# Performance work log

Hardware: AMD Instinct MI355X
Metric: run time of the kernel (lower is better)

## Reference

```python
import jax, jax.numpy as jnp
import numpy as np
from jax import lax

B = 8192; LE = 40; LD = 12; PQ = 237; IN = PQ + 19; H = 64


def setup_inputs() -> dict:
    key = jax.random.key(0)
    ks = jax.random.split(key, 26)
    def n(k, shape, s=0.05):
        return jax.random.normal(k, shape, jnp.float32) * s
    return {
        "input_p_q": jax.random.normal(ks[0], (B, LE, PQ), jnp.float32),
        "label_p": jax.random.normal(ks[1], (B, LE), jnp.float32),
        "emb_hour": n(ks[2], (24, 5)),
        "emb_weekday": n(ks[3], (8, 3)),
        "emb_month": n(ks[4], (13, 4)),
        "emb_woy": n(ks[5], (54, 7)),
        "Wi_w": n(ks[6], (H, IN)), "Wi_b": n(ks[7], (H,)),
        "We_w": n(ks[8], (H, 2 * H)),
        "Vd_w": n(ks[9], (IN, H)), "Vd_b": n(ks[10], (IN,)),
        "enc_Wih": n(ks[11], (4 * H, IN)), "enc_Whh": n(ks[12], (4 * H, H)),
        "enc_bih": n(ks[13], (4 * H,)), "enc_bhh": n(ks[14], (4 * H,)),
        "Wd_w": n(ks[15], (H, H)), "Wd_b": n(ks[16], (H,)),
        "Wd2_w": n(ks[17], (H, 2)),
        "Vdt_w": n(ks[18], (1, H)), "Vdt_b": n(ks[19], (1,)),
        "dec_Wih": n(ks[20], (4, H + 1)), "dec_Whh": n(ks[21], (4, 1)),
        "dec_bih": n(ks[22], (4,)), "dec_bhh": n(ks[23], (4,)),
        "input_time": jax.random.randint(ks[24], (B, LE, 4), 0, 8),
        "decoder_time": jax.random.randint(ks[25], (B, LD), 0, 24),
    }


def _lstm_cell(x, h, c, Wih, Whh, bih, bhh):
    # PyTorch LSTMCell gate order: i, f, g, o
    g = x @ Wih.T + bih + h @ Whh.T + bhh
    i, f, gg, o = jnp.split(g, 4, axis=1)
    c = jax.nn.sigmoid(f) * c + jax.nn.sigmoid(i) * jnp.tanh(gg)
    h = jax.nn.sigmoid(o) * jnp.tanh(c)
    return h, c


def _forward(input_p_q, label_p, emb_hour, emb_weekday, emb_month, emb_woy,
             Wi_w, Wi_b, We_w, Vd_w, Vd_b,
             enc_Wih, enc_Whh, enc_bih, enc_bhh,
             Wd_w, Wd_b, Wd2_w, Vdt_w, Vdt_b,
             dec_Wih, dec_Whh, dec_bih, dec_bhh, input_time):
    b = input_p_q.shape[0]
    inputs = jnp.concatenate([
        input_p_q,
        emb_hour[input_time[:, :, 0]],
        emb_weekday[input_time[:, :, 1]],
        emb_month[input_time[:, :, 2]],
        emb_woy[input_time[:, :, 3]],
    ], axis=2)  # [B, LE, IN]

    def enc_step(carry, x_t):
        h, c = carry
        score = jnp.tanh(jnp.concatenate([h, c], 1) @ We_w.T
                         + x_t @ Wi_w.T + Wi_b) @ Vd_w.T + Vd_b  # [B, IN]
        x_in = x_t * jax.nn.softmax(score, axis=1)
        h, c = _lstm_cell(x_in, h, c, enc_Wih, enc_Whh, enc_bih, enc_bhh)
        return (h, c), h

    z = jnp.zeros((b, H), inputs.dtype)
    _, mid = lax.scan(enc_step, (z, z), jnp.swapaxes(inputs, 0, 1))
    mid_output = jnp.swapaxes(mid, 0, 1)  # [B, LE, H]

    wd_mid = mid_output @ Wd_w.T + Wd_b  # precompute Wd(mid_output), [B, LE, H]
    dec_p_in = label_p[:, LE - 1:LE]  # [B, 1], held constant across decode steps

    def dec_step(carry, _):
        hi, ci = carry  # [B, 1] each
        q = jnp.concatenate([hi, ci], 1) @ Wd2_w.T  # [B, H]
        score = jnp.tanh(q[:, None, :] + wd_mid) @ Vdt_w.T + Vdt_b  # [B, LE, 1] (no softmax, as in source)
        ctx = jnp.einsum('bt,btd->bd', score[..., 0], mid_output)  # [B, H]
        hi, ci = _lstm_cell(jnp.concatenate([ctx, dec_p_in], 1), hi, ci,
                            dec_Wih, dec_Whh, dec_bih, dec_bhh)
        return (hi, ci), hi

    z1 = jnp.zeros((b, 1), inputs.dtype)
    _, outs = lax.scan(dec_step, (z1, z1), None, length=LD)  # [LD, B, 1]
    return jnp.swapaxes(outs[..., 0], 0, 1)  # [B, LD]


def reference(input_p_q, label_p, emb_hour, emb_weekday, emb_month, emb_woy,
              Wi_w, Wi_b, We_w, Vd_w, Vd_b,
              enc_Wih, enc_Whh, enc_bih, enc_bhh,
              Wd_w, Wd_b, Wd2_w, Vdt_w, Vdt_b,
              dec_Wih, dec_Whh, dec_bih, dec_bhh, input_time, decoder_time):
    # decoder_time is accepted by the original forward but never used
    return _forward(input_p_q, label_p, emb_hour, emb_weekday, emb_month, emb_woy,
                    Wi_w, Wi_b, We_w, Vd_w, Vd_b,
                    enc_Wih, enc_Whh, enc_bih, enc_bhh,
                    Wd_w, Wd_b, Wd2_w, Vdt_w, Vdt_b,
                    dec_Wih, dec_Whh, dec_bih, dec_bhh, input_time)
```

## Files before the change

kernel.cpp:

```cpp
#include <hip/hip_runtime.h>

#define BB   8192
#define LEN  40
#define LDN  12
#define PQN  237
#define INN  256
#define HN   64
#define BT   32
#define ENC_BLOCKS (BB / BT)
#define DW   8
#define DEC_BLOCKS (BB / DW)
#define XPS  256

typedef unsigned int  u32;
typedef _Float16 f16;
typedef f16  half8 __attribute__((ext_vector_type(8)));
typedef f16  f16x4 __attribute__((ext_vector_type(4)));
typedef float f32x4 __attribute__((ext_vector_type(4)));

#define XS 264
#define HS 72

#define OFF_WI   0
#define OFF_WE   16384
#define OFF_VD   24576
#define OFF_WIH  40960
#define OFF_WHH  106496
#define OFF_WD   122880
#define W_TOTAL  126976

#define T_H   0
#define T_W   120
#define T_M   144
#define T_Y   196
#define T_TOT 574

#define PREP_BLOCKS (BB * LEN / 32)
#define CONV_BLOCKS ((W_TOTAL + 255) / 256)

__device__ __forceinline__ float rcp_(float x){
#if __has_builtin(__builtin_amdgcn_rcpf)
  return __builtin_amdgcn_rcpf(x);
#else
  return 1.0f / x;
#endif
}
__device__ __forceinline__ float sigm(float x){
  return rcp_(1.0f + exp2f(-1.44269504f * x));
}
__device__ __forceinline__ float tanhf_(float x){
  float e = exp2f(2.88539008f * x);
  return 1.0f - 2.0f * rcp_(e + 1.0f);
}

__device__ __forceinline__ void bar_lds(){
  asm volatile("s_waitcnt lgkmcnt(0)" ::: "memory");
  __builtin_amdgcn_s_barrier();
  asm volatile("" ::: "memory");
}

__global__ __launch_bounds__(256) void conv_w(
    const float* __restrict__ Wi, const float* __restrict__ We,
    const float* __restrict__ Vd, const float* __restrict__ Wih,
    const float* __restrict__ Whh, const float* __restrict__ Wd,
    f16* __restrict__ dst)
{
  int i = blockIdx.x * 256 + threadIdx.x;
  if (i >= W_TOTAL) return;
  float v;
  if      (i < OFF_WE)  v = Wi [i - OFF_WI ];
  else if (i < OFF_VD)  v = We [i - OFF_WE ];
  else if (i < OFF_WIH) v = Vd [i - OFF_VD ];
  else if (i < OFF_WHH) v = Wih[i - OFF_WIH];
  else if (i < OFF_WD)  v = Whh[i - OFF_WHH];
  else                  v = Wd [i - OFF_WD ];
  dst[i] = (f16)v;
}

__global__ __launch_bounds__(256) void prep_all(
    const float* __restrict__ ipq,
    const float* __restrict__ e_h, const float* __restrict__ e_w,
    const float* __restrict__ e_m, const float* __restrict__ e_y,
    const int*  __restrict__ itime,
    f16* __restrict__ xpre,
    const float* __restrict__ Wi, const float* __restrict__ We,
    const float* __restrict__ Vd, const float* __restrict__ Wih,
    const float* __restrict__ Whh, const float* __restrict__ Wd,
    f16* __restrict__ wdst)
{
  if (blockIdx.x >= PREP_BLOCKS) {
    int i = (blockIdx.x - PREP_BLOCKS) * 256 + threadIdx.x;
    if (i >= W_TOTAL) return;
    float v;
    if      (i < OFF_WE)  v = Wi [i - OFF_WI ];
    else if (i < OFF_VD)  v = We [i - OFF_WE ];
    else if (i < OFF_WIH) v = Vd [i - OFF_VD ];
    else if (i < OFF_WHH) v = Wih[i - OFF_WIH];
    else if (i < OFF_WD)  v = Whh[i - OFF_WHH];
    else                  v = Wd [i - OFF_WD ];
    wdst[i] = (f16)v;
    return;
  }
  const int wv = threadIdx.x >> 6, l = threadIdx.x & 63;
  const size_t row0 = (size_t)blockIdx.x * 32 + (size_t)wv * 8;
  int4 itv[8];
  #pragma unroll
  for (int r = 0; r < 8; ++r)
    itv[r] = *(const int4*)(itime + (row0 + r) * 4);
  #pragma unroll
  for (int r = 0; r < 8; ++r) {
    const size_t row = row0 + r;
    const float* src = ipq + row * PQN;
    f16* dst = xpre + row * XPS;
    #pragma unroll
    for (int k = 0; k < 3; ++k) {
      const int c = k * 64 + l;
      dst[c] = (f16)src[c];
    }
    {
      const int c = 192 + l;
      float v;
      if (c < PQN) v = src[c];
      else {
        const int o = c - PQN;
        if      (o < 5 ) v = e_h[itv[r].x * 5 + o];
        else if (o < 8 ) v = e_w[itv[r].y * 3 + (o - 5)];
        else if (o < 12) v = e_m[itv[r].z * 4 + (o - 8)];
        else             v = e_y[itv[r].w * 7 + (o - 12)];
      }
      dst[c] = (f16)v;
    }
  }
}

__global__ __launch_bounds__(256, 1) void enc_x(
    const f16* __restrict__ xpre,
    const float* __restrict__ Wi_b,
    const float* __restrict__ Vd_b,
    const float* __restrict__ ebih, const float* __restrict__ ebhh,
    const float* __restrict__ Wd_b,
    const f16*  __restrict__ wAll,
    f16* __restrict__ xout)
{
  __shared__ __attribute__((aligned(16))) f16 Xl[2][BT * XS];
  __shared__ __attribute__((aligned(16))) f16 Ul[BT * HS];
  __shared__ __attribute__((aligned(16))) f16 Hl[2][BT * HS];
  __shared__ __attribute__((aligned(16))) f16 Cl[2][BT * HS];
  __shared__ __attribute__((aligned(16))) f16 Wml[BT * HS];
  __shared__ float Sred[2 * 64];

  const int tid  = threadIdx.x;
  const int w    = tid >> 6;
  const int lane = tid & 63;
  const int nl   = lane & 15;
  const int q    = lane >> 4;
  const int b0   = blockIdx.x * BT;
  const int d0   = w * 16 + q * 4;

  const int r0  = tid >> 5;
  const int off = tid & 31;
  const f16* gb = xpre + ((size_t)(b0 + r0) * LEN) * XPS + off * 8;
  const u32 lw0 = (u32)(r0 * XS + off * 8);

  const int orow = tid >> 3;
  const int oc8  = (tid & 7) * 8;

  half8 sr[4];
  #pragma unroll
  for (int j = 0; j < 4; ++j)
    sr[j] = *(const half8*)(gb + (size_t)(8 * j) * LEN * XPS);

  half8 wif[8], wef[4], vdf[4][2], whf[4][8], whhf[4][2], wdf[2];
  {
    const f16* pw = wAll + OFF_WI + (w * 16 + nl) * 256 + q * 8;
    #pragma unroll
    for (int kt = 0; kt < 8; ++kt) wif[kt] = *(const half8*)(pw + kt * 32);
    const f16* pe = wAll + OFF_WE + (w * 16 + nl) * 128 + q * 8;
    #pragma unroll
    for (int kt = 0; kt < 4; ++kt) wef[kt] = *(const half8*)(pe + kt * 32);
    #pragma unroll
    for (int i = 0; i < 4; ++i) {
      const f16* pv = wAll + OFF_VD + ((w + 4*i) * 16 + nl) * 64 + q * 8;
      #pragma unroll
      for (int kt = 0; kt < 2; ++kt) vdf[i][kt] = *(const half8*)(pv + kt * 32);
      const f16* ph = wAll + OFF_WIH + ((w + 4*i) * 16 + nl) * 256 + q * 8;
      #pragma unroll
      for (int kt = 0; kt < 8; ++kt) whf[i][kt] = *(const half8*)(ph + kt * 32);
      const f16* pq = wAll + OFF_WHH + ((w + 4*i) * 16 + nl) * 64 + q * 8;
      #pragma unroll
      for (int kt = 0; kt < 2; ++kt) whhf[i][kt] = *(const half8*)(pq + kt * 32);
    }
    const f16* pd = wAll + OFF_WD + (w * 16 + nl) * 64 + q * 8;
    #pragma unroll
    for (int kt = 0; kt < 2; ++kt) wdf[kt] = *(const half8*)(pd + kt * 32);
  }

  float wib[4], vdb[16], ebs[16], wdb[4];
  #pragma unroll
  for (int r = 0; r < 4; ++r) { wib[r] = Wi_b[d0 + r]; wdb[r] = Wd_b[d0 + r]; }
  #pragma unroll
  for (int i = 0; i < 4; ++i)
    #pragma unroll
    for (int r = 0; r < 4; ++r) {
      vdb[i*4+r] = Vd_b[(w + 4*i) * 16 + q * 4 + r];
      ebs[i*4+r] = ebih[i * 64 + d0 + r] + ebhh[i * 64 + d0 + r];
    }

  for (int i = tid; i < BT * HS; i += 256) {
    Hl[0][i] = (f16)0.f; Cl[0][i] = (f16)0.f;
  }
  float creg[2][4];
  #pragma unroll
  for (int bt = 0; bt < 2; ++bt)
    #pragma unroll
    for (int r = 0; r < 4; ++r) creg[bt][r] = 0.f;
  bar_lds();

  for (int t = 0; t < LEN; ++t) {
    const int cur = t & 1, nxt = cur ^ 1;
    #pragma unroll
    for (int j = 0; j < 4; ++j)
      *(half8*)(&Xl[cur][lw0 + j * 8 * XS]) = sr[j];
    if (t + 1 < LEN) {
      const f16* gp = gb + (size_t)(t + 1) * XPS;
      #pragma unroll
      for (int j = 0; j < 4; ++j)
        sr[j] = *(const half8*)(gp + (size_t)(8 * j) * LEN * XPS);
    }
    bar_lds();

    #pragma unroll
    for (int bt = 0; bt < 2; ++bt) {
      const int row = bt * 16 + nl;
      f32x4 acc = {0.f, 0.f, 0.f, 0.f};
      const f16* xb = &Xl[cur][row * XS + q * 8];
      #pragma unroll
      for (int kt = 0; kt < 8; ++kt)
        acc = __builtin_amdgcn_mfma_f32_16x16x32_f16(wif[kt], *(const half8*)(xb + kt * 32), acc, 0, 0, 0);
      const f16* hb = &Hl[cur][row * HS + q * 8];
      const f16* cb = &Cl[cur][row * HS + q * 8];
      half8 h0 = *(const half8*)hb, h1 = *(const half8*)(hb + 32);
      half8 c0 = *(const half8*)cb, c1 = *(const half8*)(cb + 32);
      acc = __builtin_amdgcn_mfma_f32_16x16x32_f16(wef[0], h0, acc, 0, 0, 0);
      acc = __builtin_amdgcn_mfma_f32_16x16x32_f16(wef[1], h1, acc, 0, 0, 0);
      acc = __builtin_amdgcn_mfma_f32_16x16x32_f16(wef[2], c0, acc, 0, 0, 0);
      acc = __builtin_amdgcn_mfma_f32_16x16x32_f16(wef[3], c1, acc, 0, 0, 0);
      f16x4 uv;
      #pragma unroll
      for (int r = 0; r < 4; ++r) uv[r] = (f16)tanhf_(acc[r] + wib[r]);
      *(f16x4*)(&Ul[row * HS + d0]) = uv;
      if (t > 0) {
        f32x4 aw = {0.f, 0.f, 0.f, 0.f};
        aw = __builtin_amdgcn_mfma_f32_16x16x32_f16(wdf[0], h0, aw, 0, 0, 0);
        aw = __builtin_amdgcn_mfma_f32_16x16x32_f16(wdf[1], h1, aw, 0, 0, 0);
        f16x4 wv;
        #pragma unroll
        for (int r = 0; r < 4; ++r) wv[r] = (f16)(aw[r] + wdb[r]);
        *(f16x4*)(&Wml[row * HS + d0]) = wv;
      }
    }
    bar_lds();

    if (t > 0) {
      half8 hv8 = *(const half8*)(&Hl[cur][orow * HS + oc8]);
      half8 wv8 = *(const half8*)(&Wml[orow * HS + oc8]);
      f16* xr = xout + ((size_t)(b0 + orow) * LEN + (t - 1)) * XPS;
      *(half8*)(xr + oc8)      = hv8;
      *(half8*)(xr + 64 + oc8) = wv8;
    }
    #pragma unroll
    for (int bt = 0; bt < 2; ++bt) {
      const int row = bt * 16 + nl;
      const f16* ub = &Ul[row * HS + q * 8];
      half8 u0 = *(const half8*)ub, u1 = *(const half8*)(ub + 32);
      float ee[16];
      #pragma unroll
      for (int i = 0; i < 4; ++i) {
        f32x4 acc = {0.f, 0.f, 0.f, 0.f};
        acc = __builtin_amdgcn_mfma_f32_16x16x32_f16(vdf[i][0], u0, acc, 0, 0, 0);
        acc = __builtin_amdgcn_mfma_f32_16x16x32_f16(vdf[i][1], u1, acc, 0, 0, 0);
        #pragma unroll
        for (int r = 0; r < 4; ++r)
          ee[i*4+r] = exp2f((acc[r] + vdb[i*4+r]) * 1.44269504f);
      }
      float s = 0.f;
      #pragma unroll
      for (int j = 0; j < 16; ++j) s += ee[j];
      s += __shfl_xor(s, 16, 64);
      s += __shfl_xor(s, 32, 64);
      if (lane < 16) Sred[bt * 64 + w * 16 + lane] = s;
      #pragma unroll
      for (int i = 0; i < 4; ++i) {
        const int k = (w + 4*i) * 16 + q * 4;
        f16x4 xv = *(const f16x4*)(&Xl[cur][row * XS + k]);
        f16x4 pv;
        #pragma unroll
        for (int r = 0; r < 4; ++r) pv[r] = (f16)((float)xv[r] * ee[i*4+r]);
        *(f16x4*)(&Xl[cur][row * XS + k]) = pv;
      }
    }
    bar_lds();

    #pragma unroll
    for (int bt = 0; bt < 2; ++bt) {
      const int row = bt * 16 + nl;
      f32x4 g[4], gh[4];
      #pragma unroll
      for (int i = 0; i < 4; ++i) {
        g[i]  = (f32x4){0.f, 0.f, 0.f, 0.f};
        gh[i] = (f32x4){0.f, 0.f, 0.f, 0.f};
      }
      const f16* pb = &Xl[cur][row * XS + q * 8];
      #pragma unroll
      for (int kt = 0; kt < 8; ++kt) {
        half8 bv = *(const half8*)(pb + kt * 32);
        #pragma unroll
        for (int i = 0; i < 4; ++i)
          g[i] = __builtin_amdgcn_mfma_f32_16x16x32_f16(whf[i][kt], bv, g[i], 0, 0, 0);
      }
      const f16* hb = &Hl[cur][row * HS + q * 8];
      half8 h0 = *(const half8*)hb, h1 = *(const half8*)(hb + 32);
      #pragma unroll
      for (int i = 0; i < 4; ++i) {
        gh[i] = __builtin_amdgcn_mfma_f32_16x16x32_f16(whhf[i][0], h0, gh[i], 0, 0, 0);
        gh[i] = __builtin_amdgcn_mfma_f32_16x16x32_f16(whhf[i][1], h1, gh[i], 0, 0, 0);
      }
      const float inv = rcp_(Sred[bt*64 + nl]      + Sred[bt*64 + 16 + nl]
                           + Sred[bt*64 + 32 + nl] + Sred[bt*64 + 48 + nl]);
      f16x4 hv, cv;
      #pragma unroll
      for (int r = 0; r < 4; ++r) {
        const float gi = g[0][r] * inv + gh[0][r] + ebs[0  + r];
        const float gf = g[1][r] * inv + gh[1][r] + ebs[4  + r];
        const float gg = g[2][r] * inv + gh[2][r] + ebs[8  + r];
        const float go = g[3][r] * inv + gh[3][r] + ebs[12 + r];
        float c = sigm(gf) * creg[bt][r] + sigm(gi) * tanhf_(gg);
        creg[bt][r] = c;
        const float h = sigm(go) * tanhf_(c);
        hv[r] = (f16)h; cv[r] = (f16)c;
      }
      *(f16x4*)(&Hl[nxt][row * HS + d0]) = hv;
      *(f16x4*)(&Cl[nxt][row * HS + d0]) = cv;
    }
  }

  bar_lds();
  #pragma unroll
  for (int bt = 0; bt < 2; ++bt) {
    const int row = bt * 16 + nl;
    const f16* hb = &Hl[0][row * HS + q * 8];
    half8 h0 = *(const half8*)hb, h1 = *(const half8*)(hb + 32);
    f32x4 aw = {0.f, 0.f, 0.f, 0.f};
    aw = __builtin_amdgcn_mfma_f32_16x16x32_f16(wdf[0], h0, aw, 0, 0, 0);
    aw = __builtin_amdgcn_mfma_f32_16x16x32_f16(wdf[1], h1, aw, 0, 0, 0);
    f16x4 wv;
    #pragma unroll
    for (int r = 0; r < 4; ++r) wv[r] = (f16)(aw[r] + wdb[r]);
    *(f16x4*)(&Wml[row * HS + d0]) = wv;
  }
  bar_lds();
  {
    half8 hv8 = *(const half8*)(&Hl[0][orow * HS + oc8]);
    half8 wv8 = *(const half8*)(&Wml[orow * HS + oc8]);
    f16* xr = xout + ((size_t)(b0 + orow) * LEN + (LEN - 1)) * XPS;
    *(half8*)(xr + oc8)      = hv8;
    *(half8*)(xr + 64 + oc8) = wv8;
  }
}

__global__ __launch_bounds__(256, 1) void enc_fb(
    const float* __restrict__ ipq,
    const float* __restrict__ e_h, const float* __restrict__ e_w,
    const float* __restrict__ e_m, const float* __restrict__ e_y,
    const float* __restrict__ Wi_b, const float* __restrict__ Vd_b,
    const float* __restrict__ ebih, const float* __restrict__ ebhh,
    const float* __restrict__ Wd_b, const f16* __restrict__ wAll,
    const int*  __restrict__ itime,
    f16* __restrict__ mid, f16* __restrict__ wmid)
{
  __shared__ __attribute__((aligned(16))) f16 Xl[BT * XS];
  __shared__ __attribute__((aligned(16))) f16 Ul[BT * HS];
  __shared__ __attribute__((aligned(16))) f16 Hl[BT * HS];
  __shared__ __attribute__((aligned(16))) f16 Cl[BT * HS];
  __shared__ float Sred[2 * 64];
  __shared__ float Tl[T_TOT];

  const int tid  = threadIdx.x;
  const int w    = tid >> 6;
  const int lane = tid & 63;
  const int nl   = lane & 15;
  const int q    = lane >> 4;
  const int b0   = blockIdx.x * BT;
  const int d0   = w * 16 + q * 4;

  const u32* pptr;
  int pstr, tstr, tbase = 0, twid = 0, tsub = 0;
  if (tid < PQN) {
    pptr = (const u32*)ipq + tid; pstr = LEN * PQN; tstr = PQN;
  } else {
    const int o = tid - PQN; int sel;
    if      (o < 5 ) { sel = 0; tbase = T_H; twid = 5; tsub = o;      }
    else if (o < 8 ) { sel = 1; tbase = T_W; twid = 3; tsub = o - 5;  }
    else if (o < 12) { sel = 2; tbase = T_M; twid = 4; tsub = o - 8;  }
    else             { sel = 3; tbase = T_Y; twid = 7; tsub = o - 12; }
    pptr = (const u32*)itime + sel; pstr = LEN * 4; tstr = 4;
  }
  pptr += (size_t)b0 * pstr;

  u32 pf[BT];
  #pragma unroll
  for (int bb = 0; bb < BT; ++bb) pf[bb] = pptr[(size_t)bb * pstr];

  half8 wif[8], wef[4], vdf[4][2], whf[4][8], whhf[4][2], wdf[2];
  {
    const f16* pw = wAll + OFF_WI + (w * 16 + nl) * 256 + q * 8;
    #pragma unroll
    for (int kt = 0; kt < 8; ++kt) wif[kt] = *(const half8*)(pw + kt * 32);
    const f16* pe = wAll + OFF_WE + (w * 16 + nl) * 128 + q * 8;
    #pragma unroll
    for (int kt = 0; kt < 4; ++kt) wef[kt] = *(const half8*)(pe + kt * 32);
    #pragma unroll
    for (int i = 0; i < 4; ++i) {
      const f16* pv = wAll + OFF_VD + ((w + 4*i) * 16 + nl) * 64 + q * 8;
      #pragma unroll
      for (int kt = 0; kt < 2; ++kt) vdf[i][kt] = *(const half8*)(pv + kt * 32);
      const f16* ph = wAll + OFF_WIH + ((w + 4*i) * 16 + nl) * 256 + q * 8;
      #pragma unroll
      for (int kt = 0; kt < 8; ++kt) whf[i][kt] = *(const half8*)(ph + kt * 32);
      const f16* pq = wAll + OFF_WHH + ((w + 4*i) * 16 + nl) * 64 + q * 8;
      #pragma unroll
      for (int kt = 0; kt < 2; ++kt) whhf[i][kt] = *(const half8*)(pq + kt * 32);
    }
    const f16* pd = wAll + OFF_WD + (w * 16 + nl) * 64 + q * 8;
    #pragma unroll
    for (int kt = 0; kt < 2; ++kt) wdf[kt] = *(const half8*)(pd + kt * 32);
  }

  float wib[4], vdb[16], ebs[16], wdb[4];
  #pragma unroll
  for (int r = 0; r < 4; ++r) { wib[r] = Wi_b[d0 + r]; wdb[r] = Wd_b[d0 + r]; }
  #pragma unroll
  for (int i = 0; i < 4; ++i)
    #pragma unroll
    for (int r = 0; r < 4; ++r) {
      vdb[i*4+r] = Vd_b[(w + 4*i) * 16 + q * 4 + r];
      ebs[i*4+r] = ebih[i * 64 + d0 + r] + ebhh[i * 64 + d0 + r];
    }

  for (int i = tid; i < BT * HS; i += 256) { Hl[i] = (f16)0.f; Cl[i] = (f16)0.f; }
  for (int i = tid; i < T_TOT; i += 256) {
    float v;
    if      (i < T_W) v = e_h[i];
    else if (i < T_M) v = e_w[i - T_W];
    else if (i < T_Y) v = e_m[i - T_M];
    else              v = e_y[i - T_Y];
    Tl[i] = v;
  }
  float creg[2][4];
  #pragma unroll
  for (int bt = 0; bt < 2; ++bt)
    #pragma unroll
    for (int r = 0; r < 4; ++r) creg[bt][r] = 0.f;
  bar_lds();

  for (int t = 0; t < LEN; ++t) {
    #pragma unroll
    for (int bb = 0; bb < BT; ++bb) {
      float v;
      if (tid < PQN) v = __uint_as_float(pf[bb]);
      else           v = Tl[tbase + (int)pf[bb] * twid + tsub];
      Xl[bb * XS + tid] = (f16)v;
    }
    if (t + 1 < LEN) {
      const u32* pp = pptr + (size_t)(t + 1) * tstr;
      #pragma unroll
      for (int bb = 0; bb < BT; ++bb) pf[bb] = pp[(size_t)bb * pstr];
    }
    bar_lds();

    #pragma unroll
    for (int bt = 0; bt < 2; ++bt) {
      const int row = bt * 16 + nl;
      f32x4 acc = {0.f, 0.f, 0.f, 0.f};
      const f16* xb = &Xl[row * XS + q * 8];
      #pragma unroll
      for (int kt = 0; kt < 8; ++kt)
        acc = __builtin_amdgcn_mfma_f32_16x16x32_f16(wif[kt], *(const half8*)(xb + kt * 32), acc, 0, 0, 0);
      const f16* hb = &Hl[row * HS + q * 8];
      const f16* cb = &Cl[row * HS + q * 8];
      half8 h0 = *(const half8*)hb, h1 = *(const half8*)(hb + 32);
      half8 c0 = *(const half8*)cb, c1 = *(const half8*)(cb + 32);
      acc = __builtin_amdgcn_mfma_f32_16x16x32_f16(wef[0], h0, acc, 0, 0, 0);
      acc = __builtin_amdgcn_mfma_f32_16x16x32_f16(wef[1], h1, acc, 0, 0, 0);
      acc = __builtin_amdgcn_mfma_f32_16x16x32_f16(wef[2], c0, acc, 0, 0, 0);
      acc = __builtin_amdgcn_mfma_f32_16x16x32_f16(wef[3], c1, acc, 0, 0, 0);
      f16x4 uv;
      #pragma unroll
      for (int r = 0; r < 4; ++r) uv[r] = (f16)tanhf_(acc[r] + wib[r]);
      *(f16x4*)(&Ul[row * HS + d0]) = uv;
      if (t > 0) {
        f32x4 aw = {0.f, 0.f, 0.f, 0.f};
        aw = __builtin_amdgcn_mfma_f32_16x16x32_f16(wdf[0], h0, aw, 0, 0, 0);
        aw = __builtin_amdgcn_mfma_f32_16x16x32_f16(wdf[1], h1, aw, 0, 0, 0);
        f16x4 wv;
        #pragma unroll
        for (int r = 0; r < 4; ++r) wv[r] = (f16)(aw[r] + wdb[r]);
        *(f16x4*)(&wmid[((size_t)(b0 + row) * LEN + (t - 1)) * HN + d0]) = wv;
      }
    }
    bar_lds();

    #pragma unroll
    for (int bt = 0; bt < 2; ++bt) {
      const int row = bt * 16 + nl;
      const f16* ub = &Ul[row * HS + q * 8];
      half8 u0 = *(const half8*)ub, u1 = *(const half8*)(ub + 32);
      float ee[16];
      #pragma unroll
      for (int i = 0; i < 4; ++i) {
        f32x4 acc = {0.f, 0.f, 0.f, 0.f};
        acc = __builtin_amdgcn_mfma_f32_16x16x32_f16(vdf[i][0], u0, acc, 0, 0, 0);
        acc = __builtin_amdgcn_mfma_f32_16x16x32_f16(vdf[i][1], u1, acc, 0, 0, 0);
        #pragma unroll
        for (int r = 0; r < 4; ++r)
          ee[i*4+r] = exp2f((acc[r] + vdb[i*4+r]) * 1.44269504f);
      }
      float s = 0.f;
      #pragma unroll
      for (int j = 0; j < 16; ++j) s += ee[j];
      s += __shfl_xor(s, 16, 64);
      s += __shfl_xor(s, 32, 64);
      if (lane < 16) Sred[bt * 64 + w * 16 + lane] = s;
      #pragma unroll
      for (int i = 0; i < 4; ++i) {
        const int k = (w + 4*i) * 16 + q * 4;
        f16x4 xv = *(const f16x4*)(&Xl[row * XS + k]);
        f16x4 pv;
        #pragma unroll
        for (int r = 0; r < 4; ++r) pv[r] = (f16)((float)xv[r] * ee[i*4+r]);
        *(f16x4*)(&Xl[row * XS + k]) = pv;
      }
    }
    bar_lds();

    f16x4 hstash[2], cstash[2];
    #pragma unroll
    for (int bt = 0; bt < 2; ++bt) {
      const int row = bt * 16 + nl;
      f32x4 g[4], gh[4];
      #pragma unroll
      for (int i = 0; i < 4; ++i) {
        g[i]  = (f32x4){0.f, 0.f, 0.f, 0.f};
        gh[i] = (f32x4){0.f, 0.f, 0.f, 0.f};
      }
      const f16* pb = &Xl[row * XS + q * 8];
      #pragma unroll
      for (int kt = 0; kt < 8; ++kt) {
        half8 bv = *(const half8*)(pb + kt * 32);
        #pragma unroll
        for (int i = 0; i < 4; ++i)
          g[i] = __builtin_amdgcn_mfma_f32_16x16x32_f16(whf[i][kt], bv, g[i], 0, 0, 0);
      }
      const f16* hb = &Hl[row * HS + q * 8];
      half8 h0 = *(const half8*)hb, h1 = *(const half8*)(hb + 32);
      #pragma unroll
      for (int i = 0; i < 4; ++i) {
        gh[i] = __builtin_amdgcn_mfma_f32_16x16x32_f16(whhf[i][0], h0, gh[i], 0, 0, 0);
        gh[i] = __builtin_amdgcn_mfma_f32_16x16x32_f16(whhf[i][1], h1, gh[i], 0, 0, 0);
      }
      const float inv = rcp_(Sred[bt*64 + nl]      + Sred[bt*64 + 16 + nl]
                           + Sred[bt*64 + 32 + nl] + Sred[bt*64 + 48 + nl]);
      f16x4 hv, cv;
      #pragma unroll
      for (int r = 0; r < 4; ++r) {
        const float gi = g[0][r] * inv + gh[0][r] + ebs[0  + r];
        const float gf = g[1][r] * inv + gh[1][r] + ebs[4  + r];
        const float gg = g[2][r] * inv + gh[2][r] + ebs[8  + r];
        const float go = g[3][r] * inv + gh[3][r] + ebs[12 + r];
        float c = sigm(gf) * creg[bt][r] + sigm(gi) * tanhf_(gg);
        creg[bt][r] = c;
        const float h = sigm(go) * tanhf_(c);
        hv[r] = (f16)h; cv[r] = (f16)c;
      }
      hstash[bt] = hv; cstash[bt] = cv;
      *(f16x4*)(&mid[((size_t)(b0 + row) * LEN + t) * HN + d0]) = hv;
    }
    bar_lds();
    #pragma unroll
    for (int bt = 0; bt < 2; ++bt) {
      const int row = bt * 16 + nl;
      *(f16x4*)(&Hl[row * HS + d0]) = hstash[bt];
      *(f16x4*)(&Cl[row * HS + d0]) = cstash[bt];
    }
  }

  bar_lds();
  #pragma unroll
  for (int bt = 0; bt < 2; ++bt) {
    const int row = bt * 16 + nl;
    const f16* hb = &Hl[row * HS + q * 8];
    half8 h0 = *(const half8*)hb, h1 = *(const half8*)(hb + 32);
    f32x4 aw = {0.f, 0.f, 0.f, 0.f};
    aw = __builtin_amdgcn_mfma_f32_16x16x32_f16(wdf[0], h0, aw, 0, 0, 0);
    aw = __builtin_amdgcn_mfma_f32_16x16x32_f16(wdf[1], h1, aw, 0, 0, 0);
    f16x4 wv;
    #pragma unroll
    for (int r = 0; r < 4; ++r) wv[r] = (f16)(aw[r] + wdb[r]);
    *(f16x4*)(&wmid[((size_t)(b0 + row) * LEN + (LEN - 1)) * HN + d0]) = wv;
  }
}

__global__ __launch_bounds__(512) void dec_kernel(
    const f16* __restrict__ mids,
    const f16* __restrict__ wms,
    const int MS,
    const float* __restrict__ lblp,
    const float* __restrict__ Wd2_w,
    const float* __restrict__ Vdt_w,
    const float* __restrict__ Vdt_b,
    const float* __restrict__ dWih,
    const float* __restrict__ dWhh,
    const float* __restrict__ dbih, const float* __restrict__ dbhh,
    float* __restrict__ out)
{
  __shared__ __attribute__((aligned(16))) float qv[DW][HN];
  __shared__ __attribute__((aligned(16))) float vs[HN];
  __shared__ __attribute__((aligned(16))) float ws4[4 * 65];

  const int w    = threadIdx.x >> 6;
  const int lane = threadIdx.x & 63;
  const int b    = blockIdx.x * DW + w;

  if (threadIdx.x < HN)     vs[threadIdx.x]  = Vdt_w[threadIdx.x];
  if (threadIdx.x < 4 * 65) ws4[threadIdx.x] = dWih[threadIdx.x];

  half8 wmr[8];
  if (lane < LEN) {
    const f16* p = wms + ((size_t)b * LEN + lane) * MS;
    #pragma unroll
    for (int k = 0; k < 8; ++k) wmr[k] = *(const half8*)(p + k * 8);
  } else {
    #pragma unroll
    for (int k = 0; k < 8; ++k)
      #pragma unroll
      for (int e = 0; e < 8; ++e) wmr[k][e] = (f16)0.f;
  }
  __syncthreads();

  float macc[4] = {0.f, 0.f, 0.f, 0.f};
  if (lane < LEN) {
    const f16* mrow = mids + ((size_t)b * LEN + lane) * MS;
    #pragma unroll
    for (int k8 = 0; k8 < 8; ++k8) {
      half8 mv = *(const half8*)(mrow + k8 * 8);
      #pragma unroll
      for (int e = 0; e < 8; ++e) {
        const float m = (float)mv[e];
        #pragma unroll
        for (int j = 0; j < 4; ++j) macc[j] += ws4[j * 65 + k8 * 8 + e] * m;
      }
    }
  }

  const float dpin = lblp[b * LEN + (LEN - 1)];
  const float w20 = Wd2_w[2 * lane];
  const float w21 = Wd2_w[2 * lane + 1];
  const float vdtb = Vdt_b[0];
  float wxx[4], whh4[4], bb4[4];
  #pragma unroll
  for (int j = 0; j < 4; ++j) {
    wxx[j]  = dWih[j * 65 + 64];
    whh4[j] = dWhh[j];
    bb4[j]  = dbih[j] + dbhh[j];
  }

  float hi = 0.0f, ci = 0.0f;
  for (int s = 0; s < LDN; ++s) {
    qv[w][lane] = w20 * hi + w21 * ci;

    float p0 = 0.f, p1 = 0.f, p2 = 0.f, p3 = 0.f;
    if (lane < LEN) {
      float acc = 0.f;
      #pragma unroll
      for (int k8 = 0; k8 < 8; ++k8) {
        float4 qa = *(const float4*)&qv[w][k8 * 8];
        float4 qb = *(const float4*)&qv[w][k8 * 8 + 4];
        float4 va = *(const float4*)&vs[k8 * 8];
        float4 vb = *(const float4*)&vs[k8 * 8 + 4];
        half8 wv = wmr[k8];
        acc += tanhf_(qa.x + (float)wv[0]) * va.x
             + tanhf_(qa.y + (float)wv[1]) * va.y
             + tanhf_(qa.z + (float)wv[2]) * va.z
             + tanhf_(qa.w + (float)wv[3]) * va.w
             + tanhf_(qb.x + (float)wv[4]) * vb.x
             + tanhf_(qb.y + (float)wv[5]) * vb.y
             + tanhf_(qb.z + (float)wv[6]) * vb.z
             + tanhf_(qb.w + (float)wv[7]) * vb.w;
      }
      const float score = acc + vdtb;
      p0 = score * macc[0]; p1 = score * macc[1];
      p2 = score * macc[2]; p3 = score * macc[3];
    }
    #pragma unroll
    for (int off = 32; off >= 1; off >>= 1) {
      p0 += __shfl_xor(p0, off, 64);
      p1 += __shfl_xor(p1, off, 64);
      p2 += __shfl_xor(p2, off, 64);
      p3 += __shfl_xor(p3, off, 64);
    }
    const float g0 = p0 + wxx[0] * dpin + bb4[0] + whh4[0] * hi;
    const float g1 = p1 + wxx[1] * dpin + bb4[1] + whh4[1] * hi;
    const float g2 = p2 + wxx[2] * dpin + bb4[2] + whh4[2] * hi;
    const float g3 = p3 + wxx[3] * dpin + bb4[3] + whh4[3] * hi;
    ci = sigm(g1) * ci + sigm(g0) * tanhf_(g2);
    hi = sigm(g3) * tanhf_(ci);
    if (lane == 0) out[b * LDN + s] = hi;
  }
}

extern "C" void kernel_launch(void* const* d_in, const int* in_sizes, int n_in,
                              void* d_out, int out_size, void* d_ws, size_t ws_size,
                              hipStream_t stream) {
  (void)in_sizes; (void)n_in; (void)out_size;
  const float* ipq   = (const float*)d_in[0];
  const float* lblp  = (const float*)d_in[1];
  const float* e_h   = (const float*)d_in[2];
  const float* e_w   = (const float*)d_in[3];
  const float* e_m   = (const float*)d_in[4];
  const float* e_y   = (const float*)d_in[5];
  const float* Wi_w  = (const float*)d_in[6];
  const float* Wi_b  = (const float*)d_in[7];
  const float* We_w  = (const float*)d_in[8];
  const float* Vd_w  = (const float*)d_in[9];
  const float* Vd_b  = (const float*)d_in[10];
  const float* eWih  = (const float*)d_in[11];
  const float* eWhh  = (const float*)d_in[12];
  const float* ebih  = (const float*)d_in[13];
  const float* ebhh  = (const float*)d_in[14];
  const float* Wd_w  = (const float*)d_in[15];
  const float* Wd_b  = (const float*)d_in[16];
  const float* Wd2_w = (const float*)d_in[17];
  const float* Vdt_w = (const float*)d_in[18];
  const float* Vdt_b = (const float*)d_in[19];
  const float* dWih  = (const float*)d_in[20];
  const float* dWhh  = (const float*)d_in[21];
  const float* dbih  = (const float*)d_in[22];
  const float* dbhh  = (const float*)d_in[23];
  const int* itime   = (const int*)d_in[24];
  float* out = (float*)d_out;

  const size_t xpreB = (size_t)BB * LEN * XPS * 2;
  const size_t wcvtB = (size_t)W_TOTAL * 2;

  if (ws_size >= xpreB + wcvtB) {
    f16* xpre = (f16*)d_ws;
    f16* wcvt = (f16*)((char*)d_ws + xpreB);
    prep_all<<<dim3(PREP_BLOCKS + CONV_BLOCKS), dim3(256), 0, stream>>>(
        ipq, e_h, e_w, e_m, e_y, itime, xpre,
        Wi_w, We_w, Vd_w, eWih, eWhh, Wd_w, wcvt);
    enc_x<<<dim3(ENC_BLOCKS), dim3(256), 0, stream>>>(
        xpre, Wi_b, Vd_b, ebih, ebhh, Wd_b, wcvt, xpre);
    dec_kernel<<<dim3(DEC_BLOCKS), dim3(512), 0, stream>>>(
        xpre, xpre + 64, XPS, lblp, Wd2_w, Vdt_w, Vdt_b,
        dWih, dWhh, dbih, dbhh, out);
  } else {
    const size_t midB = (size_t)BB * LEN * HN * 2;
    f16* mid  = (f16*)d_ws;
    f16* wmid = (f16*)((char*)d_ws + midB);
    f16* wcvt = (f16*)((char*)d_ws + 2 * midB);
    conv_w<<<dim3(CONV_BLOCKS), dim3(256), 0, stream>>>(
        Wi_w, We_w, Vd_w, eWih, eWhh, Wd_w, wcvt);
    enc_fb<<<dim3(ENC_BLOCKS), dim3(256), 0, stream>>>(
        ipq, e_h, e_w, e_m, e_y, Wi_b, Vd_b, ebih, ebhh, Wd_b, wcvt, itime,
        mid, wmid);
    dec_kernel<<<dim3(DEC_BLOCKS), dim3(512), 0, stream>>>(
        mid, wmid, HN, lblp, Wd2_w, Vdt_w, Vdt_b,
        dWih, dWhh, dbih, dbhh, out);
  }
}
```

Before: 876.3 us.

## Split encoder batch halves across 8 waves and stage small weights in LDS

The encoder kernel now runs 512 threads per block instead of 256. Each group of four waves handles one 16-row half of the batch tile instead of looping over both halves. The We, Vd, Whh and Wd weight fragments and the bias vectors move from registers into shared memory, and launch bounds become (512,2). This cuts per-thread register pressure and raises occupancy and wave-level parallelism for the latency-bound recurrent loop, at the cost of extra LDS reads per MFMA and more shared memory per block.

Measured after the change: 882.4 us. About the same (+0.7%).

```diff
diff --git a/kernel.cpp b/kernel.cpp
--- a/kernel.cpp
+++ b/kernel.cpp
@@ -133,7 +133,7 @@
   }
 }
 
-__global__ __launch_bounds__(256, 1) void enc_x(
+__global__ __launch_bounds__(512, 2) void enc_x(
     const f16* __restrict__ xpre,
     const float* __restrict__ Wi_b,
     const float* __restrict__ Vd_b,
@@ -148,90 +148,94 @@
   __shared__ __attribute__((aligned(16))) f16 Cl[2][BT * HS];
   __shared__ __attribute__((aligned(16))) f16 Wml[BT * HS];
   __shared__ float Sred[2 * 64];
+  __shared__ __attribute__((aligned(16))) f16 WeL[4 * 4 * 64 * 8];
+  __shared__ __attribute__((aligned(16))) f16 VdL[16 * 2 * 64 * 8];
+  __shared__ __attribute__((aligned(16))) f16 WhL[16 * 2 * 64 * 8];
+  __shared__ __attribute__((aligned(16))) f16 WdL[4 * 2 * 64 * 8];
+  __shared__ float VdbL[256];
+  __shared__ float EbsL[256];
 
   const int tid  = threadIdx.x;
   const int w    = tid >> 6;
   const int lane = tid & 63;
   const int nl   = lane & 15;
   const int q    = lane >> 4;
+  const int wsub = w & 3;
+  const int bt   = w >> 2;
   const int b0   = blockIdx.x * BT;
-  const int d0   = w * 16 + q * 4;
+  const int d0   = wsub * 16 + q * 4;
+  const int row  = bt * 16 + nl;
 
   const int r0  = tid >> 5;
   const int off = tid & 31;
-  const f16* gb = xpre + ((size_t)(b0 + r0) * LEN) * XPS + off * 8;
-  const u32 lw0 = (u32)(r0 * XS + off * 8);
-
-  const int orow = tid >> 3;
-  const int oc8  = (tid & 7) * 8;
-
-  half8 sr[4];
-  #pragma unroll
-  for (int j = 0; j < 4; ++j)
-    sr[j] = *(const half8*)(gb + (size_t)(8 * j) * LEN * XPS);
-
-  half8 wif[8], wef[4], vdf[4][2], whf[4][8], whhf[4][2], wdf[2];
+  const f16* gb0 = xpre + ((size_t)(b0 + r0     ) * LEN) * XPS + off * 8;
+  const f16* gb1 = xpre + ((size_t)(b0 + r0 + 16) * LEN) * XPS + off * 8;
+  const u32 lwa = (u32)(r0 * XS + off * 8);
+  const u32 lwb = (u32)((r0 + 16) * XS + off * 8);
+
+  const int orow = tid >> 4;
+  const int oc8  = (tid & 15) * 8;
+
+  half8 sr0 = *(const half8*)gb0;
+  half8 sr1 = *(const half8*)gb1;
+
+  half8 wif[8], whf[4][8];
   {
-    const f16* pw = wAll + OFF_WI + (w * 16 + nl) * 256 + q * 8;
+    const f16* pw = wAll + OFF_WI + (wsub * 16 + nl) * 256 + q * 8;
     #pragma unroll
     for (int kt = 0; kt < 8; ++kt) wif[kt] = *(const half8*)(pw + kt * 32);
-    const f16* pe = wAll + OFF_WE + (w * 16 + nl) * 128 + q * 8;
-    #pragma unroll
-    for (int kt = 0; kt < 4; ++kt) wef[kt] = *(const half8*)(pe + kt * 32);
     #pragma unroll
     for (int i = 0; i < 4; ++i) {
-      const f16* pv = wAll + OFF_VD + ((w + 4*i) * 16 + nl) * 64 + q * 8;
-      #pragma unroll
-      for (int kt = 0; kt < 2; ++kt) vdf[i][kt] = *(const half8*)(pv + kt * 32);
-      const f16* ph = wAll + OFF_WIH + ((w + 4*i) * 16 + nl) * 256 + q * 8;
+      const f16* ph = wAll + OFF_WIH + ((wsub + 4*i) * 16 + nl) * 256 + q * 8;
       #pragma unroll
       for (int kt = 0; kt < 8; ++kt) whf[i][kt] = *(const half8*)(ph + kt * 32);
-      const f16* pq = wAll + OFF_WHH + ((w + 4*i) * 16 + nl) * 64 + q * 8;
-      #pragma unroll
-      for (int kt = 0; kt < 2; ++kt) whhf[i][kt] = *(const half8*)(pq + kt * 32);
-    }
-    const f16* pd = wAll + OFF_WD + (w * 16 + nl) * 64 + q * 8;
-    #pragma unroll
-    for (int kt = 0; kt < 2; ++kt) wdf[kt] = *(const half8*)(pd + kt * 32);
-  }
-
-  float wib[4], vdb[16], ebs[16], wdb[4];
+    }
+  }
+  float wib[4], wdb[4];
   #pragma unroll
   for (int r = 0; r < 4; ++r) { wib[r] = Wi_b[d0 + r]; wdb[r] = Wd_b[d0 + r]; }
-  #pragma unroll
-  for (int i = 0; i < 4; ++i)
-    #pragma unroll
-    for (int r = 0; r < 4; ++r) {
-      vdb[i*4+r] = Vd_b[(w + 4*i) * 16 + q * 4 + r];
-      ebs[i*4+r] = ebih[i * 64 + d0 + r] + ebhh[i * 64 + d0 + r];
-    }
-
-  for (int i = tid; i < BT * HS; i += 256) {
+
+  for (int s = tid; s < 4 * 4 * 64; s += 512) {
+    const int tile = s >> 8, kt = (s >> 6) & 3, ln = s & 63;
+    *(half8*)(&WeL[(size_t)s * 8]) = *(const half8*)(
+        wAll + OFF_WE + (tile * 16 + (ln & 15)) * 128 + (ln >> 4) * 8 + kt * 32);
+  }
+  for (int s = tid; s < 16 * 2 * 64; s += 512) {
+    const int tile = s >> 7, kt = (s >> 6) & 1, ln = s & 63;
+    *(half8*)(&VdL[(size_t)s * 8]) = *(const half8*)(
+        wAll + OFF_VD + (tile * 16 + (ln & 15)) * 64 + (ln >> 4) * 8 + kt * 32);
+  }
+  for (int s = tid; s < 16 * 2 * 64; s += 512) {
+    const int tile = s >> 7, kt = (s >> 6) & 1, ln = s & 63;
+    *(half8*)(&WhL[(size_t)s * 8]) = *(const half8*)(
+        wAll + OFF_WHH + (tile * 16 + (ln & 15)) * 64 + (ln >> 4) * 8 + kt * 32);
+  }
+  for (int s = tid; s < 4 * 2 * 64; s += 512) {
+    const int tile = s >> 7, kt = (s >> 6) & 1, ln = s & 63;
+    *(half8*)(&WdL[(size_t)s * 8]) = *(const half8*)(
+        wAll + OFF_WD + (tile * 16 + (ln & 15)) * 64 + (ln >> 4) * 8 + kt * 32);
+  }
+  if (tid < 256) {
+    VdbL[tid] = Vd_b[tid];
+    EbsL[tid] = ebih[tid] + ebhh[tid];
+  }
+  for (int i = tid; i < BT * HS; i += 512) {
     Hl[0][i] = (f16)0.f; Cl[0][i] = (f16)0.f;
   }
-  float creg[2][4];
-  #pragma unroll
-  for (int bt = 0; bt < 2; ++bt)
-    #pragma unroll
-    for (int r = 0; r < 4; ++r) creg[bt][r] = 0.f;
+  float creg[4] = {0.f, 0.f, 0.f, 0.f};
   bar_lds();
 
   for (int t = 0; t < LEN; ++t) {
     const int cur = t & 1, nxt = cur ^ 1;
-    #pragma unroll
-    for (int j = 0; j < 4; ++j)
-      *(half8*)(&Xl[cur][lw0 + j * 8 * XS]) = sr[j];
+    *(half8*)(&Xl[cur][lwa]) = sr0;
+    *(half8*)(&Xl[cur][lwb]) = sr1;
     if (t + 1 < LEN) {
-      const f16* gp = gb + (size_t)(t + 1) * XPS;
-      #pragma unroll
-      for (int j = 0; j < 4; ++j)
-        sr[j] = *(const half8*)(gp + (size_t)(8 * j) * LEN * XPS);
+      sr0 = *(const half8*)(gb0 + (size_t)(t + 1) * XPS);
+      sr1 = *(const half8*)(gb1 + (size_t)(t + 1) * XPS);
     }
     bar_lds();
 
-    #pragma unroll
-    for (int bt = 0; bt < 2; ++bt) {
-      const int row = bt * 16 + nl;
+    {
       f32x4 acc = {0.f, 0.f, 0.f, 0.f};
       const f16* xb = &Xl[cur][row * XS + q * 8];
       #pragma unroll
@@ -241,18 +245,24 @@
       const f16* cb = &Cl[cur][row * HS + q * 8];
       half8 h0 = *(const half8*)hb, h1 = *(const half8*)(hb + 32);
       half8 c0 = *(const half8*)cb, c1 = *(const half8*)(cb + 32);
-      acc = __builtin_amdgcn_mfma_f32_16x16x32_f16(wef[0], h0, acc, 0, 0, 0);
-      acc = __builtin_amdgcn_mfma_f32_16x16x32_f16(wef[1], h1, acc, 0, 0, 0);
-      acc = __builtin_amdgcn_mfma_f32_16x16x32_f16(wef[2], c0, acc, 0, 0, 0);
-      acc = __builtin_amdgcn_mfma_f32_16x16x32_f16(wef[3], c1, acc, 0, 0, 0);
+      acc = __builtin_amdgcn_mfma_f32_16x16x32_f16(
+          *(const half8*)(&WeL[((wsub * 4 + 0) * 64 + lane) * 8]), h0, acc, 0, 0, 0);
+      acc = __builtin_amdgcn_mfma_f32_16x16x32_f16(
+          *(const half8*)(&WeL[((wsub * 4 + 1) * 64 + lane) * 8]), h1, acc, 0, 0, 0);
+      acc = __builtin_amdgcn_mfma_f32_16x16x32_f16(
+          *(const half8*)(&WeL[((wsub * 4 + 2) * 64 + lane) * 8]), c0, acc, 0, 0, 0);
+      acc = __builtin_amdgcn_mfma_f32_16x16x32_f16(
+          *(const half8*)(&WeL[((wsub * 4 + 3) * 64 + lane) * 8]), c1, acc, 0, 0, 0);
       f16x4 uv;
       #pragma unroll
       for (int r = 0; r < 4; ++r) uv[r] = (f16)tanhf_(acc[r] + wib[r]);
       *(f16x4*)(&Ul[row * HS + d0]) = uv;
       if (t > 0) {
         f32x4 aw = {0.f, 0.f, 0.f, 0.f};
-        aw = __builtin_amdgcn_mfma_f32_16x16x32_f16(wdf[0], h0, aw, 0, 0, 0);
-        aw = __builtin_amdgcn_mfma_f32_16x16x32_f16(wdf[1], h1, aw, 0, 0, 0);
+        aw = __builtin_amdgcn_mfma_f32_16x16x32_f16(
+            *(const half8*)(&WdL[((wsub * 2 + 0) * 64 + lane) * 8]), h0, aw, 0, 0, 0);
+        aw = __builtin_amdgcn_mfma_f32_16x16x32_f16(
+            *(const half8*)(&WdL[((wsub * 2 + 1) * 64 + lane) * 8]), h1, aw, 0, 0, 0);
         f16x4 wv;
         #pragma unroll
         for (int r = 0; r < 4; ++r) wv[r] = (f16)(aw[r] + wdb[r]);
@@ -262,48 +272,42 @@
     bar_lds();
 
     if (t > 0) {
-      half8 hv8 = *(const half8*)(&Hl[cur][orow * HS + oc8]);
-      half8 wv8 = *(const half8*)(&Wml[orow * HS + oc8]);
-      f16* xr = xout + ((size_t)(b0 + orow) * LEN + (t - 1)) * XPS;
-      *(half8*)(xr + oc8)      = hv8;
-      *(half8*)(xr + 64 + oc8) = wv8;
-    }
-    #pragma unroll
-    for (int bt = 0; bt < 2; ++bt) {
-      const int row = bt * 16 + nl;
+      const f16* srcp = (oc8 < 64) ? &Hl[cur][orow * HS + oc8]
+                                   : &Wml[orow * HS + (oc8 - 64)];
+      half8 v8 = *(const half8*)srcp;
+      *(half8*)(xout + ((size_t)(b0 + orow) * LEN + (t - 1)) * XPS + oc8) = v8;
+    }
+    {
       const f16* ub = &Ul[row * HS + q * 8];
       half8 u0 = *(const half8*)ub, u1 = *(const half8*)(ub + 32);
-      float ee[16];
+      float s = 0.f;
       #pragma unroll
       for (int i = 0; i < 4; ++i) {
+        const int tile = wsub + 4 * i;
         f32x4 acc = {0.f, 0.f, 0.f, 0.f};
-        acc = __builtin_amdgcn_mfma_f32_16x16x32_f16(vdf[i][0], u0, acc, 0, 0, 0);
-        acc = __builtin_amdgcn_mfma_f32_16x16x32_f16(vdf[i][1], u1, acc, 0, 0, 0);
+        acc = __builtin_amdgcn_mfma_f32_16x16x32_f16(
+            *(const half8*)(&VdL[((tile * 2 + 0) * 64 + lane) * 8]), u0, acc, 0, 0, 0);
+        acc = __builtin_amdgcn_mfma_f32_16x16x32_f16(
+            *(const half8*)(&VdL[((tile * 2 + 1) * 64 + lane) * 8]), u1, acc, 0, 0, 0);
+        const int k = tile * 16 + q * 4;
+        f16x4 xv = *(const f16x4*)(&Xl[cur][row * XS + k]);
+        f16x4 pv;
+        float ee[4];
         #pragma unroll
-        for (int r = 0; r < 4; ++r)
-          ee[i*4+r] = exp2f((acc[r] + vdb[i*4+r]) * 1.44269504f);
-      }
-      float s = 0.f;
-      #pragma unroll
-      for (int j = 0; j < 16; ++j) s += ee[j];
+        for (int r = 0; r < 4; ++r) {
+          ee[r] = exp2f((acc[r] + VdbL[k + r]) * 1.44269504f);
+          s += ee[r];
+          pv[r] = (f16)((float)xv[r] * ee[r]);
+        }
+        *(f16x4*)(&Xl[cur][row * XS + k]) = pv;
+      }
       s += __shfl_xor(s, 16, 64);
       s += __shfl_xor(s, 32, 64);
-      if (lane < 16) Sred[bt * 64 + w * 16 + lane] = s;
-      #pragma unroll
-      for (int i = 0; i < 4; ++i) {
-        const int k = (w + 4*i) * 16 + q * 4;
-        f16x4 xv = *(const f16x4*)(&Xl[cur][row * XS + k]);
-        f16x4 pv;
-        #pragma unroll
-        for (int r = 0; r < 4; ++r) pv[r] = (f16)((float)xv[r] * ee[i*4+r]);
-        *(f16x4*)(&Xl[cur][row * XS + k]) = pv;
-      }
+      if (lane < 16) Sred[bt * 64 + wsub * 16 + lane] = s;
     }
     bar_lds();
 
-    #pragma unroll
-    for (int bt = 0; bt < 2; ++bt) {
-      const int row = bt * 16 + nl;
+    {
       f32x4 g[4], gh[4];
       #pragma unroll
       for (int i = 0; i < 4; ++i) {
@@ -322,20 +326,23 @@
       half8 h0 = *(const half8*)hb, h1 = *(const half8*)(hb + 32);
       #pragma unroll
       for (int i = 0; i < 4; ++i) {
-        gh[i] = __builtin_amdgcn_mfma_f32_16x16x32_f16(whhf[i][0], h0, gh[i], 0, 0, 0);
-        gh[i] = __builtin_amdgcn_mfma_f32_16x16x32_f16(whhf[i][1], h1, gh[i], 0, 0, 0);
+        const int tile = wsub + 4 * i;
+        gh[i] = __builtin_amdgcn_mfma_f32_16x16x32_f16(
+            *(const half8*)(&WhL[((tile * 2 + 0) * 64 + lane) * 8]), h0, gh[i], 0, 0, 0);
+        gh[i] = __builtin_amdgcn_mfma_f32_16x16x32_f16(
+            *(const half8*)(&WhL[((tile * 2 + 1) * 64 + lane) * 8]), h1, gh[i], 0, 0, 0);
       }
       const float inv = rcp_(Sred[bt*64 + nl]      + Sred[bt*64 + 16 + nl]
                            + Sred[bt*64 + 32 + nl] + Sred[bt*64 + 48 + nl]);
       f16x4 hv, cv;
       #pragma unroll
       for (int r = 0; r < 4; ++r) {
-        const float gi = g[0][r] * inv + gh[0][r] + ebs[0  + r];
-        const float gf = g[1][r] * inv + gh[1][r] + ebs[4  + r];
-        const float gg = g[2][r] * inv + gh[2][r] + ebs[8  + r];
-        const float go = g[3][r] * inv + gh[3][r] + ebs[12 + r];
-        float c = sigm(gf) * creg[bt][r] + sigm(gi) * tanhf_(gg);
-        creg[bt][r] = c;
+        const float gi = g[0][r] * inv + gh[0][r] + EbsL[0   + d0 + r];
+        const float gf = g[1][r] * inv + gh[1][r] + EbsL[64  + d0 + r];
+        const float gg = g[2][r] * inv + gh[2][r] + EbsL[128 + d0 + r];
+        const float go = g[3][r] * inv + gh[3][r] + EbsL[192 + d0 + r];
+        float c = sigm(gf) * creg[r] + sigm(gi) * tanhf_(gg);
+        creg[r] = c;
         const float h = sigm(go) * tanhf_(c);
         hv[r] = (f16)h; cv[r] = (f16)c;
       }
@@ -345,14 +352,14 @@
   }
 
   bar_lds();
-  #pragma unroll
-  for (int bt = 0; bt < 2; ++bt) {
-    const int row = bt * 16 + nl;
+  {
     const f16* hb = &Hl[0][row * HS + q * 8];
     half8 h0 = *(const half8*)hb, h1 = *(const half8*)(hb + 32);
     f32x4 aw = {0.f, 0.f, 0.f, 0.f};
-    aw = __builtin_amdgcn_mfma_f32_16x16x32_f16(wdf[0], h0, aw, 0, 0, 0);
-    aw = __builtin_amdgcn_mfma_f32_16x16x32_f16(wdf[1], h1, aw, 0, 0, 0);
+    aw = __builtin_amdgcn_mfma_f32_16x16x32_f16(
+        *(const half8*)(&WdL[((wsub * 2 + 0) * 64 + lane) * 8]), h0, aw, 0, 0, 0);
+    aw = __builtin_amdgcn_mfma_f32_16x16x32_f16(
+        *(const half8*)(&WdL[((wsub * 2 + 1) * 64 + lane) * 8]), h1, aw, 0, 0, 0);
     f16x4 wv;
     #pragma unroll
     for (int r = 0; r < 4; ++r) wv[r] = (f16)(aw[r] + wdb[r]);
@@ -360,11 +367,10 @@
   }
   bar_lds();
   {
-    half8 hv8 = *(const half8*)(&Hl[0][orow * HS + oc8]);
-    half8 wv8 = *(const half8*)(&Wml[orow * HS + oc8]);
-    f16* xr = xout + ((size_t)(b0 + orow) * LEN + (LEN - 1)) * XPS;
-    *(half8*)(xr + oc8)      = hv8;
-    *(half8*)(xr + 64 + oc8) = wv8;
+    const f16* srcp = (oc8 < 64) ? &Hl[0][orow * HS + oc8]
+                                 : &Wml[orow * HS + (oc8 - 64)];
+    half8 v8 = *(const half8*)srcp;
+    *(half8*)(xout + ((size_t)(b0 + orow) * LEN + (LEN - 1)) * XPS + oc8) = v8;
   }
 }
 
@@ -758,7 +764,7 @@
     prep_all<<<dim3(PREP_BLOCKS + CONV_BLOCKS), dim3(256), 0, stream>>>(
         ipq, e_h, e_w, e_m, e_y, itime, xpre,
         Wi_w, We_w, Vd_w, eWih, eWhh, Wd_w, wcvt);
-    enc_x<<<dim3(ENC_BLOCKS), dim3(256), 0, stream>>>(
+    enc_x<<<dim3(ENC_BLOCKS), dim3(512), 0, stream>>>(
         xpre, Wi_b, Vd_b, ebih, ebhh, Wd_b, wcvt, xpre);
     dec_kernel<<<dim3(DEC_BLOCKS), dim3(512), 0, stream>>>(
         xpre, xpre + 64, XPS, lblp, Wd2_w, Vdt_w, Vdt_b,
```
